# Kernel tuning notes

Measured on AMD Instinct MI355X. Metric: run time of the kernel, lower is better.

Reference implementation:

```python
import jax, jax.numpy as jnp
import numpy as np

B, S, D = 2, 2048, 1024
H = 16
HD = D // H

def setup_inputs() -> dict:
    key = jax.random.key(0)
    k1, k2, k3 = jax.random.split(key, 3)
    x = jax.random.normal(k1, (B, S, D), dtype=jnp.float32)
    w_attn = jax.random.normal(k2, (D, 3 * D), dtype=jnp.float32) * (1.0 / np.sqrt(D))
    b_attn = jnp.zeros((3 * D,), dtype=jnp.float32)
    w_proj = jax.random.normal(k3, (D, D), dtype=jnp.float32) * (1.0 / np.sqrt(D))
    b_proj = jnp.zeros((D,), dtype=jnp.float32)
    return {"x": x, "w_attn": w_attn, "b_attn": b_attn, "w_proj": w_proj, "b_proj": b_proj}

def reference(x, w_attn, b_attn, w_proj, b_proj):
    bsz, seq_len, embed_dim = x.shape
    qkv = x @ w_attn + b_attn                      # [B,S,3D]
    q, k, v = jnp.split(qkv, 3, axis=-1)
    # [B,S,D] -> [B,H,S,HD]
    def heads(t):
        return t.reshape(bsz, seq_len, H, HD).transpose(0, 2, 1, 3)
    q, k, v = heads(q), heads(k), heads(v)
    scale = 1.0 / np.sqrt(HD)
    att = jnp.einsum('bhqd,bhkd->bhqk', q, k) * scale  # [B,H,S,S]
    causal = jnp.tril(jnp.ones((seq_len, seq_len), dtype=bool))
    att = jnp.where(causal[None, None], att, jnp.float32(-jnp.inf))
    att = jax.nn.softmax(att, axis=-1)
    y = jnp.einsum('bhqk,bhkd->bhqd', att, v)          # [B,H,S,HD]
    y = y.transpose(0, 2, 1, 3).reshape(bsz, seq_len, embed_dim)
    return y @ w_proj + b_proj
```

## Files before the change

kernel.cpp:

```cpp
#include <hip/hip_runtime.h>
#include <hip/hip_bf16.h>
#include <math.h>

typedef __bf16 bf16x8 __attribute__((ext_vector_type(8)));
typedef __bf16 bf16x4 __attribute__((ext_vector_type(4)));
typedef float f32x4 __attribute__((ext_vector_type(4)));

#define LOG2E 1.44269504088896340736f

#define SEQ 2048
#define DMODEL 1024
#define NH 16
#define HD 64

__device__ __forceinline__ void gl2lds16(const void* g, void* l) {
  __builtin_amdgcn_global_load_lds((__attribute__((address_space(1))) void*)g,
                                   (__attribute__((address_space(3))) void*)l,
                                   16, 0, 0);
}

__device__ __forceinline__ unsigned compute_flag_local(const unsigned* __restrict__ x,
                                                       int* cnt) {
  int c = 0;
  for (int i = threadIdx.x; i < 4096; i += 256) {
    unsigned e = (x[i] >> 23) & 0xFF;
    c += (e >= 0x70 && e <= 0x8F) ? 1 : 0;
  }
#pragma unroll
  for (int o = 32; o > 0; o >>= 1) c += __shfl_xor(c, o, 64);
  if ((threadIdx.x & 63) == 0) cnt[threadIdx.x >> 6] = c;
  __syncthreads();
  const int tot = cnt[0] + cnt[1] + cnt[2] + cnt[3];
  return (tot > 2048) ? 1u : 0u;
}

__device__ __forceinline__ void transpose_tile(const void* __restrict__ in,
                                               __hip_bfloat16* __restrict__ out,
                                               int R, int C, int c0, int r0, bool f32,
                                               __hip_bfloat16 (*tile)[65]) {
  const int tx = threadIdx.x & 63, ty = threadIdx.x >> 6;
#pragma unroll
  for (int i = 0; i < 16; ++i) {
    int r = ty + i * 4;
    long idx = (long)(r0 + r) * C + c0 + tx;
    tile[r][tx] = f32 ? __float2bfloat16(((const float*)in)[idx])
                      : ((const __hip_bfloat16*)in)[idx];
  }
  __syncthreads();
#pragma unroll
  for (int i = 0; i < 16; ++i) {
    int r = ty + i * 4;
    out[(long)(c0 + r) * R + r0 + tx] = tile[tx][r];
  }
}

__global__ void prep_all(const void* __restrict__ x, const void* __restrict__ w_attn,
                         const void* __restrict__ w_proj,
                         __hip_bfloat16* __restrict__ x_bf,
                         __hip_bfloat16* __restrict__ wT_attn,
                         __hip_bfloat16* __restrict__ wT_proj,
                         unsigned* __restrict__ flag) {
  __shared__ int cnt[4];
  __shared__ __hip_bfloat16 tile[64][65];
  const unsigned f = compute_flag_local((const unsigned*)x, cnt);
  const int bid = blockIdx.x;
  if (bid == 0 && threadIdx.x == 0) flag[0] = f;

  if (bid < 4096) {
    const int i = (bid * 256 + threadIdx.x) * 4;
    if (f) {
      const float4 v = *(const float4*)((const float*)x + i);
      x_bf[i + 0] = __float2bfloat16(v.x);
      x_bf[i + 1] = __float2bfloat16(v.y);
      x_bf[i + 2] = __float2bfloat16(v.z);
      x_bf[i + 3] = __float2bfloat16(v.w);
    } else {
      *(bf16x4*)(x_bf + i) = *(const bf16x4*)((const __hip_bfloat16*)x + i);
    }
  } else if (bid < 4096 + 768) {
    const int b2 = bid - 4096;
    const int c0 = (b2 % 48) * 64, r0 = (b2 / 48) * 64;
    transpose_tile(w_attn, wT_attn, 1024, 3072, c0, r0, f != 0, tile);
  } else {
    const int b3 = bid - 4096 - 768;
    const int c0 = (b3 % 16) * 64, r0 = (b3 / 16) * 64;
    transpose_tile(w_proj, wT_proj, 1024, 1024, c0, r0, f != 0, tile);
  }
}

template <int MODE, int BN>
__global__ __launch_bounds__(256, BN == 128 ? 3 : (BN == 64 ? 6 : 4)) void gemm_bt(
    const __hip_bfloat16* __restrict__ A, const __hip_bfloat16* __restrict__ Bt,
    const void* __restrict__ bias, void* __restrict__ C,
    __hip_bfloat16* __restrict__ q_ws, __hip_bfloat16* __restrict__ k_ws,
    __hip_bfloat16* __restrict__ vt_ws, int M, int N, int K,
    const unsigned* __restrict__ flag) {
  constexpr int NJ = BN / 32;
  alignas(16) __shared__ __hip_bfloat16 lA[128 * 64];
  alignas(16) __shared__ __hip_bfloat16 lB[BN * 64];
  const int tid = threadIdx.x;
  const int wave = tid >> 6, lane = tid & 63;
  const int l15 = lane & 15, lq = lane >> 4;
  const int m0 = blockIdx.y * 128, n0 = blockIdx.x * BN;
  const int wrow = (wave >> 1) * 64, wcol = (wave & 1) * (BN / 2);

  const int rs = lane >> 3;
  const int cs = lane & 7;
  const int gch = cs ^ rs;
  const __hip_bfloat16* ap0 = A + (long)(m0 + wave * 32 + rs) * K + gch * 8;
  const __hip_bfloat16* bp0 = Bt + (long)(n0 + wave * (BN / 4) + rs) * K + gch * 8;

  f32x4 acc[4][NJ];
#pragma unroll
  for (int i = 0; i < 4; ++i)
#pragma unroll
    for (int j = 0; j < NJ; ++j) acc[i][j] = {0.f, 0.f, 0.f, 0.f};

  for (int k0 = 0; k0 < K; k0 += 64) {
    __syncthreads();
#pragma unroll
    for (int i = 0; i < 4; ++i)
      gl2lds16(ap0 + (long)(i * 8) * K + k0, lA + (wave * 4 + i) * 512);
#pragma unroll
    for (int i = 0; i < NJ; ++i)
      gl2lds16(bp0 + (long)(i * 8) * K + k0, lB + (wave * NJ + i) * 512);
    __syncthreads();
#pragma unroll
    for (int ks = 0; ks < 2; ++ks) {
      bf16x8 af[4], bfr[NJ];
#pragma unroll
      for (int i = 0; i < 4; ++i) {
        const int p = wrow + 16 * i + l15;
        af[i] = *(const bf16x8*)(lA + p * 64 + (((ks * 4 + lq) ^ (l15 & 7)) * 8));
      }
#pragma unroll
      for (int j = 0; j < NJ; ++j) {
        const int p = wcol + 16 * j + l15;
        bfr[j] = *(const bf16x8*)(lB + p * 64 + (((ks * 4 + lq) ^ (l15 & 7)) * 8));
      }
#pragma unroll
      for (int i = 0; i < 4; ++i)
#pragma unroll
        for (int j = 0; j < NJ; ++j)
          acc[i][j] = __builtin_amdgcn_mfma_f32_16x16x32_bf16(af[i], bfr[j], acc[i][j], 0, 0, 0);
    }
  }

  const bool f32in = (*flag != 0);
  const bool outf32 = (MODE == 0) && f32in;
  const float KSCL = 0.125f * LOG2E;
#pragma unroll
  for (int i = 0; i < 4; ++i) {
    const int row = m0 + wrow + 16 * i + lq * 4;
#pragma unroll
    for (int j = 0; j < NJ; ++j) {
      const int col = n0 + wcol + 16 * j + l15;
      const float bv = f32in ? ((const float*)bias)[col]
                             : __bfloat162float(((const __hip_bfloat16*)bias)[col]);
#pragma unroll
      for (int r = 0; r < 4; ++r) {
        const float v = acc[i][j][r] + bv;
        const int rr = row + r;
        if (MODE == 0) {
          if (outf32)
            ((float*)C)[(long)rr * N + col] = v;
          else
            ((__hip_bfloat16*)C)[(long)rr * N + col] = __float2bfloat16(v);
        } else {
          const int which = col >> 10;
          const int f = col & 1023;
          const int h = f >> 6, d = f & 63;
          const int b = rr >> 11, s = rr & 2047;
          const long bh = (long)b * NH + h;
          if (which == 0)
            q_ws[(bh * SEQ + s) * HD + d] = __float2bfloat16(v);
          else if (which == 1)
            k_ws[(bh * SEQ + s) * HD + d] = __float2bfloat16(v * KSCL);
          else {
            const int w = s & 31;
            const int wl = w & 15;
            const int sig = (w >> 4) ? (2 * (wl & ~3) + 4 + (wl & 3))
                                     : (2 * (wl & ~3) + (wl & 3));
            const int sp = (s & ~31) | sig;
            vt_ws[(bh * HD + d) * SEQ + sp] = __float2bfloat16(v);
          }
        }
      }
    }
  }
}

__global__ __launch_bounds__(256, 4) void attn_fused(
    const __hip_bfloat16* __restrict__ q_ws, const __hip_bfloat16* __restrict__ k_ws,
    const __hip_bfloat16* __restrict__ vt_ws, __hip_bfloat16* __restrict__ y_ws) {
  alignas(16) __shared__ __hip_bfloat16 lK[2][64 * 64];
  alignas(16) __shared__ __hip_bfloat16 lV[2][64 * 64];
  const int tid = threadIdx.x, wave = tid >> 6, lane = tid & 63;
  const int l15 = lane & 15, lq = lane >> 4;
  const int qt = 31 - (blockIdx.x >> 5);
  const int bh = blockIdx.x & 31;
  const int q0 = qt * 64;
  const int nkt = qt + 1;
  const __hip_bfloat16* Qb = q_ws + (long)bh * SEQ * HD;
  const __hip_bfloat16* Kb = k_ws + (long)bh * SEQ * HD;
  const __hip_bfloat16* Vb = vt_ws + (long)bh * HD * SEQ;
  const int b = bh >> 4, h = bh & 15;

  const int qrow = q0 + wave * 16 + l15;
  const bf16x8 qa0 = *(const bf16x8*)(Qb + (long)qrow * HD + lq * 8);
  const bf16x8 qa1 = *(const bf16x8*)(Qb + (long)qrow * HD + 32 + lq * 8);

  f32x4 accO[4];
  f32x4 accL;
#pragma unroll
  for (int j = 0; j < 4; ++j) accO[j] = {0.f, 0.f, 0.f, 0.f};
  accL = {0.f, 0.f, 0.f, 0.f};
  const __bf16 one = (__bf16)1.0f;
  const bf16x8 onesA = {one, one, one, one, one, one, one, one};

  const int p0 = wave * 16 + (lane >> 3);
  const int cl = lane & 7;
  const __hip_bfloat16* kpre[2];
  const __hip_bfloat16* vpre[2];

#pragma unroll
  for (int i = 0; i < 2; ++i) {
    const int p = p0 + i * 8;
    const int c = cl ^ (p & 7);
    kpre[i] = Kb + (long)p * HD + c * 8;
    vpre[i] = Vb + (long)p * SEQ + c * 8;
    gl2lds16(kpre[i], &lK[0][(wave * 16 + i * 8) * 64]);
    gl2lds16(vpre[i], &lV[0][(wave * 16 + i * 8) * 64]);
    kpre[i] += 64 * HD;
    vpre[i] += 64;
  }
  __syncthreads();

#pragma unroll 1
  for (int kt = 0; kt < nkt; ++kt) {
    const int buf = kt & 1;
    if (kt + 1 < nkt) {
#pragma unroll
      for (int i = 0; i < 2; ++i) {
        gl2lds16(kpre[i], &lK[buf ^ 1][(wave * 16 + i * 8) * 64]);
        gl2lds16(vpre[i], &lV[buf ^ 1][(wave * 16 + i * 8) * 64]);
        kpre[i] += 64 * HD;
        vpre[i] += 64;
      }
    }
    const __hip_bfloat16* lKb = lK[buf];
    const __hip_bfloat16* lVb = lV[buf];

    f32x4 st[4];
    __builtin_amdgcn_s_setprio(1);
#pragma unroll
    for (int t = 0; t < 4; ++t) {
      st[t] = {0.f, 0.f, 0.f, 0.f};
      const int pp = t * 16 + l15;
      const bf16x8 kb0 = *(const bf16x8*)(lKb + (pp * 8 + (lq ^ (pp & 7))) * 8);
      const bf16x8 kb1 = *(const bf16x8*)(lKb + (pp * 8 + ((4 + lq) ^ (pp & 7))) * 8);
      st[t] = __builtin_amdgcn_mfma_f32_16x16x32_bf16(kb0, qa0, st[t], 0, 0, 0);
      st[t] = __builtin_amdgcn_mfma_f32_16x16x32_bf16(kb1, qa1, st[t], 0, 0, 0);
    }
    __builtin_amdgcn_s_setprio(0);

    const bool diag = (kt == nkt - 1);
    const int qloc = wave * 16 + l15;
    bf16x8 pb[2];
#pragma unroll
    for (int c = 0; c < 2; ++c) {
#pragma unroll
      for (int t2 = 0; t2 < 2; ++t2) {
        const int tt = c * 2 + t2;
#pragma unroll
        for (int r = 0; r < 4; ++r) {
          float pv = exp2f(st[tt][r]);
          if (diag) {
            const int colloc = tt * 16 + lq * 4 + r;
            pv = (colloc <= qloc) ? pv : 0.f;
          }
          pb[c][t2 * 4 + r] = (__bf16)pv;
        }
      }
    }

    __builtin_amdgcn_s_setprio(1);
#pragma unroll
    for (int j = 0; j < 4; ++j) {
      const int d = j * 16 + l15;
      const bf16x8 va0 = *(const bf16x8*)(lVb + (d * 8 + (lq ^ (d & 7))) * 8);
      const bf16x8 va1 = *(const bf16x8*)(lVb + (d * 8 + ((4 + lq) ^ (d & 7))) * 8);
      accO[j] = __builtin_amdgcn_mfma_f32_16x16x32_bf16(va0, pb[0], accO[j], 0, 0, 0);
      accO[j] = __builtin_amdgcn_mfma_f32_16x16x32_bf16(va1, pb[1], accO[j], 0, 0, 0);
    }
    accL = __builtin_amdgcn_mfma_f32_16x16x32_bf16(onesA, pb[0], accL, 0, 0, 0);
    accL = __builtin_amdgcn_mfma_f32_16x16x32_bf16(onesA, pb[1], accL, 0, 0, 0);
    __builtin_amdgcn_s_setprio(0);
    __syncthreads();
  }

  const float inv = 1.f / accL[0];
  const int s = q0 + wave * 16 + l15;
  __hip_bfloat16* yb = y_ws + (long)(b * SEQ + s) * DMODEL + h * HD;
#pragma unroll
  for (int j = 0; j < 4; ++j) {
    bf16x4 o;
#pragma unroll
    for (int r = 0; r < 4; ++r) o[r] = (__bf16)(accO[j][r] * inv);
    *(bf16x4*)(yb + j * 16 + lq * 4) = o;
  }
}

extern "C" void kernel_launch(void* const* d_in, const int* in_sizes, int n_in,
                              void* d_out, int out_size, void* d_ws, size_t ws_size,
                              hipStream_t stream) {
  const void* x = d_in[0];
  const void* w_attn = d_in[1];
  const void* b_attn = d_in[2];
  const void* w_proj = d_in[3];
  const void* b_proj = d_in[4];

  char* ws = (char*)d_ws;
  const size_t MB = 1024 * 1024;
  unsigned* flag = (unsigned*)ws;
  __hip_bfloat16* wT_attn = (__hip_bfloat16*)(ws + 1 * MB);
  __hip_bfloat16* wT_proj = (__hip_bfloat16*)(ws + 7 * MB);
  __hip_bfloat16* x_bf = (__hip_bfloat16*)(ws + 9 * MB);
  __hip_bfloat16* q_ws = (__hip_bfloat16*)(ws + 17 * MB);
  __hip_bfloat16* k_ws = (__hip_bfloat16*)(ws + 25 * MB);
  __hip_bfloat16* vt_ws = (__hip_bfloat16*)(ws + 33 * MB);
  __hip_bfloat16* y_ws = (__hip_bfloat16*)(ws + 41 * MB);

  prep_all<<<dim3(4096 + 768 + 256), 256, 0, stream>>>(
      x, w_attn, w_proj, x_bf, wT_attn, wT_proj, flag);

  gemm_bt<1, 64><<<dim3(3072 / 64, 4096 / 128), 256, 0, stream>>>(
      x_bf, wT_attn, b_attn, nullptr, q_ws, k_ws, vt_ws, 4096, 3072, 1024, flag);

  attn_fused<<<dim3(1024), 256, 0, stream>>>(q_ws, k_ws, vt_ws, y_ws);

  gemm_bt<0, 32><<<dim3(1024 / 32, 4096 / 128), 256, 0, stream>>>(
      y_ws, wT_proj, b_proj, d_out, nullptr, nullptr, nullptr, 4096, 1024, 1024, flag);
}
```

Before: 194.6 us.

## Use 128-row query tiles with 512-thread attention blocks and retune prep and proj GEMM

Result: no change. 192.6 us (-1.0%).

```diff
diff --git a/kernel.cpp b/kernel.cpp
--- a/kernel.cpp
+++ b/kernel.cpp
@@ -66,30 +66,33 @@
   const int bid = blockIdx.x;
   if (bid == 0 && threadIdx.x == 0) flag[0] = f;
 
-  if (bid < 4096) {
-    const int i = (bid * 256 + threadIdx.x) * 4;
-    if (f) {
-      const float4 v = *(const float4*)((const float*)x + i);
-      x_bf[i + 0] = __float2bfloat16(v.x);
-      x_bf[i + 1] = __float2bfloat16(v.y);
-      x_bf[i + 2] = __float2bfloat16(v.z);
-      x_bf[i + 3] = __float2bfloat16(v.w);
-    } else {
-      *(bf16x4*)(x_bf + i) = *(const bf16x4*)((const __hip_bfloat16*)x + i);
-    }
-  } else if (bid < 4096 + 768) {
-    const int b2 = bid - 4096;
+  if (bid < 1024) {
+#pragma unroll
+    for (int rep = 0; rep < 4; ++rep) {
+      const int i = ((bid * 4 + rep) * 256 + threadIdx.x) * 4;
+      if (f) {
+        const float4 v = *(const float4*)((const float*)x + i);
+        x_bf[i + 0] = __float2bfloat16(v.x);
+        x_bf[i + 1] = __float2bfloat16(v.y);
+        x_bf[i + 2] = __float2bfloat16(v.z);
+        x_bf[i + 3] = __float2bfloat16(v.w);
+      } else {
+        *(bf16x4*)(x_bf + i) = *(const bf16x4*)((const __hip_bfloat16*)x + i);
+      }
+    }
+  } else if (bid < 1024 + 768) {
+    const int b2 = bid - 1024;
     const int c0 = (b2 % 48) * 64, r0 = (b2 / 48) * 64;
     transpose_tile(w_attn, wT_attn, 1024, 3072, c0, r0, f != 0, tile);
   } else {
-    const int b3 = bid - 4096 - 768;
+    const int b3 = bid - 1024 - 768;
     const int c0 = (b3 % 16) * 64, r0 = (b3 / 16) * 64;
     transpose_tile(w_proj, wT_proj, 1024, 1024, c0, r0, f != 0, tile);
   }
 }
 
 template <int MODE, int BN>
-__global__ __launch_bounds__(256, BN == 128 ? 3 : (BN == 64 ? 6 : 4)) void gemm_bt(
+__global__ __launch_bounds__(256, BN == 128 ? 3 : 6) void gemm_bt(
     const __hip_bfloat16* __restrict__ A, const __hip_bfloat16* __restrict__ Bt,
     const void* __restrict__ bias, void* __restrict__ C,
     __hip_bfloat16* __restrict__ q_ws, __hip_bfloat16* __restrict__ k_ws,
@@ -190,17 +193,19 @@
   }
 }
 
-__global__ __launch_bounds__(256, 4) void attn_fused(
+__global__ __launch_bounds__(512, 4) void attn_fused(
     const __hip_bfloat16* __restrict__ q_ws, const __hip_bfloat16* __restrict__ k_ws,
     const __hip_bfloat16* __restrict__ vt_ws, __hip_bfloat16* __restrict__ y_ws) {
   alignas(16) __shared__ __hip_bfloat16 lK[2][64 * 64];
   alignas(16) __shared__ __hip_bfloat16 lV[2][64 * 64];
   const int tid = threadIdx.x, wave = tid >> 6, lane = tid & 63;
   const int l15 = lane & 15, lq = lane >> 4;
-  const int qt = 31 - (blockIdx.x >> 5);
+  const int grp = blockIdx.x >> 5;
   const int bh = blockIdx.x & 31;
-  const int q0 = qt * 64;
-  const int nkt = qt + 1;
+  const int qt = (grp < 8) ? (15 - grp) : (grp - 8);
+  const int q0 = qt * 128;
+  const int nkt = 2 * qt + 2;
+  const int myLast = nkt - 2 + (wave >> 2);
   const __hip_bfloat16* Qb = q_ws + (long)bh * SEQ * HD;
   const __hip_bfloat16* Kb = k_ws + (long)bh * SEQ * HD;
   const __hip_bfloat16* Vb = vt_ws + (long)bh * HD * SEQ;
@@ -218,84 +223,76 @@
   const __bf16 one = (__bf16)1.0f;
   const bf16x8 onesA = {one, one, one, one, one, one, one, one};
 
-  const int p0 = wave * 16 + (lane >> 3);
-  const int cl = lane & 7;
-  const __hip_bfloat16* kpre[2];
-  const __hip_bfloat16* vpre[2];
-
-#pragma unroll
-  for (int i = 0; i < 2; ++i) {
-    const int p = p0 + i * 8;
-    const int c = cl ^ (p & 7);
-    kpre[i] = Kb + (long)p * HD + c * 8;
-    vpre[i] = Vb + (long)p * SEQ + c * 8;
-    gl2lds16(kpre[i], &lK[0][(wave * 16 + i * 8) * 64]);
-    gl2lds16(vpre[i], &lV[0][(wave * 16 + i * 8) * 64]);
-    kpre[i] += 64 * HD;
-    vpre[i] += 64;
-  }
+  const int p0 = wave * 8 + (lane >> 3);
+  const int c = (lane & 7) ^ (p0 & 7);
+  const __hip_bfloat16* kpre = Kb + (long)p0 * HD + c * 8;
+  const __hip_bfloat16* vpre = Vb + (long)p0 * SEQ + c * 8;
+
+  gl2lds16(kpre, &lK[0][(wave * 8) * 64]);
+  gl2lds16(vpre, &lV[0][(wave * 8) * 64]);
+  kpre += 64 * HD;
+  vpre += 64;
   __syncthreads();
 
 #pragma unroll 1
   for (int kt = 0; kt < nkt; ++kt) {
     const int buf = kt & 1;
     if (kt + 1 < nkt) {
-#pragma unroll
-      for (int i = 0; i < 2; ++i) {
-        gl2lds16(kpre[i], &lK[buf ^ 1][(wave * 16 + i * 8) * 64]);
-        gl2lds16(vpre[i], &lV[buf ^ 1][(wave * 16 + i * 8) * 64]);
-        kpre[i] += 64 * HD;
-        vpre[i] += 64;
-      }
-    }
-    const __hip_bfloat16* lKb = lK[buf];
-    const __hip_bfloat16* lVb = lV[buf];
-
-    f32x4 st[4];
-    __builtin_amdgcn_s_setprio(1);
-#pragma unroll
-    for (int t = 0; t < 4; ++t) {
-      st[t] = {0.f, 0.f, 0.f, 0.f};
-      const int pp = t * 16 + l15;
-      const bf16x8 kb0 = *(const bf16x8*)(lKb + (pp * 8 + (lq ^ (pp & 7))) * 8);
-      const bf16x8 kb1 = *(const bf16x8*)(lKb + (pp * 8 + ((4 + lq) ^ (pp & 7))) * 8);
-      st[t] = __builtin_amdgcn_mfma_f32_16x16x32_bf16(kb0, qa0, st[t], 0, 0, 0);
-      st[t] = __builtin_amdgcn_mfma_f32_16x16x32_bf16(kb1, qa1, st[t], 0, 0, 0);
-    }
-    __builtin_amdgcn_s_setprio(0);
-
-    const bool diag = (kt == nkt - 1);
-    const int qloc = wave * 16 + l15;
-    bf16x8 pb[2];
-#pragma unroll
-    for (int c = 0; c < 2; ++c) {
-#pragma unroll
-      for (int t2 = 0; t2 < 2; ++t2) {
-        const int tt = c * 2 + t2;
-#pragma unroll
-        for (int r = 0; r < 4; ++r) {
-          float pv = exp2f(st[tt][r]);
-          if (diag) {
-            const int colloc = tt * 16 + lq * 4 + r;
-            pv = (colloc <= qloc) ? pv : 0.f;
+      gl2lds16(kpre, &lK[buf ^ 1][(wave * 8) * 64]);
+      gl2lds16(vpre, &lV[buf ^ 1][(wave * 8) * 64]);
+      kpre += 64 * HD;
+      vpre += 64;
+    }
+    if (kt <= myLast) {
+      const __hip_bfloat16* lKb = lK[buf];
+      const __hip_bfloat16* lVb = lV[buf];
+
+      f32x4 st[4];
+      __builtin_amdgcn_s_setprio(1);
+#pragma unroll
+      for (int t = 0; t < 4; ++t) {
+        st[t] = {0.f, 0.f, 0.f, 0.f};
+        const int pp = t * 16 + l15;
+        const bf16x8 kb0 = *(const bf16x8*)(lKb + (pp * 8 + (lq ^ (pp & 7))) * 8);
+        const bf16x8 kb1 = *(const bf16x8*)(lKb + (pp * 8 + ((4 + lq) ^ (pp & 7))) * 8);
+        st[t] = __builtin_amdgcn_mfma_f32_16x16x32_bf16(kb0, qa0, st[t], 0, 0, 0);
+        st[t] = __builtin_amdgcn_mfma_f32_16x16x32_bf16(kb1, qa1, st[t], 0, 0, 0);
+      }
+      __builtin_amdgcn_s_setprio(0);
+
+      const bool diag = (kt == myLast);
+      const int qloc = (wave & 3) * 16 + l15;
+      bf16x8 pb[2];
+#pragma unroll
+      for (int cc = 0; cc < 2; ++cc) {
+#pragma unroll
+        for (int t2 = 0; t2 < 2; ++t2) {
+          const int tt = cc * 2 + t2;
+#pragma unroll
+          for (int r = 0; r < 4; ++r) {
+            float pv = exp2f(st[tt][r]);
+            if (diag) {
+              const int colloc = tt * 16 + lq * 4 + r;
+              pv = (colloc <= qloc) ? pv : 0.f;
+            }
+            pb[cc][t2 * 4 + r] = (__bf16)pv;
           }
-          pb[c][t2 * 4 + r] = (__bf16)pv;
         }
       }
-    }
-
-    __builtin_amdgcn_s_setprio(1);
-#pragma unroll
-    for (int j = 0; j < 4; ++j) {
-      const int d = j * 16 + l15;
-      const bf16x8 va0 = *(const bf16x8*)(lVb + (d * 8 + (lq ^ (d & 7))) * 8);
-      const bf16x8 va1 = *(const bf16x8*)(lVb + (d * 8 + ((4 + lq) ^ (d & 7))) * 8);
-      accO[j] = __builtin_amdgcn_mfma_f32_16x16x32_bf16(va0, pb[0], accO[j], 0, 0, 0);
-      accO[j] = __builtin_amdgcn_mfma_f32_16x16x32_bf16(va1, pb[1], accO[j], 0, 0, 0);
-    }
-    accL = __builtin_amdgcn_mfma_f32_16x16x32_bf16(onesA, pb[0], accL, 0, 0, 0);
-    accL = __builtin_amdgcn_mfma_f32_16x16x32_bf16(onesA, pb[1], accL, 0, 0, 0);
-    __builtin_amdgcn_s_setprio(0);
+
+      __builtin_amdgcn_s_setprio(1);
+#pragma unroll
+      for (int j = 0; j < 4; ++j) {
+        const int d = j * 16 + l15;
+        const bf16x8 va0 = *(const bf16x8*)(lVb + (d * 8 + (lq ^ (d & 7))) * 8);
+        const bf16x8 va1 = *(const bf16x8*)(lVb + (d * 8 + ((4 + lq) ^ (d & 7))) * 8);
+        accO[j] = __builtin_amdgcn_mfma_f32_16x16x32_bf16(va0, pb[0], accO[j], 0, 0, 0);
+        accO[j] = __builtin_amdgcn_mfma_f32_16x16x32_bf16(va1, pb[1], accO[j], 0, 0, 0);
+      }
+      accL = __builtin_amdgcn_mfma_f32_16x16x32_bf16(onesA, pb[0], accL, 0, 0, 0);
+      accL = __builtin_amdgcn_mfma_f32_16x16x32_bf16(onesA, pb[1], accL, 0, 0, 0);
+      __builtin_amdgcn_s_setprio(0);
+    }
     __syncthreads();
   }
 
@@ -331,14 +328,14 @@
   __hip_bfloat16* vt_ws = (__hip_bfloat16*)(ws + 33 * MB);
   __hip_bfloat16* y_ws = (__hip_bfloat16*)(ws + 41 * MB);
 
-  prep_all<<<dim3(4096 + 768 + 256), 256, 0, stream>>>(
+  prep_all<<<dim3(1024 + 768 + 256), 256, 0, stream>>>(
       x, w_attn, w_proj, x_bf, wT_attn, wT_proj, flag);
 
   gemm_bt<1, 64><<<dim3(3072 / 64, 4096 / 128), 256, 0, stream>>>(
       x_bf, wT_attn, b_attn, nullptr, q_ws, k_ws, vt_ws, 4096, 3072, 1024, flag);
 
-  attn_fused<<<dim3(1024), 256, 0, stream>>>(q_ws, k_ws, vt_ws, y_ws);
-
-  gemm_bt<0, 32><<<dim3(1024 / 32, 4096 / 128), 256, 0, stream>>>(
+  attn_fused<<<dim3(512), 512, 0, stream>>>(q_ws, k_ws, vt_ws, y_ws);
+
+  gemm_bt<0, 64><<<dim3(1024 / 64, 4096 / 128), 256, 0, stream>>>(
       y_ws, wT_proj, b_proj, d_out, nullptr, nullptr, nullptr, 4096, 1024, 1024, flag);
 }
```
